# Kernel optimization log

Hardware: AMD Instinct MI355X
Metric: run time of the kernel (lower is better)

## Reference

```python
import jax, jax.numpy as jnp
import numpy as np

DOWN = 8
N_CLASSES = 80
IOU_THRESH = 0.7
ALL_ANCHORS = np.array([[10, 13], [16, 30], [33, 23], [30, 61], [62, 45],
                        [59, 119], [116, 90], [156, 198], [373, 326]],
                       np.float32) / DOWN              # anchors in grid units
ANCHOR_IDX = np.array([0, 1, 2])
ANCHORS = ALL_ANCHORS[ANCHOR_IDX]                       # [A,2]
A = 3
NC = N_CLASSES + 5


def _clog(z):
    # torch BCE clamps log at -100; double-where keeps grads finite at z==0
    safe = jnp.where(z > 0, z, 1.0)
    return jnp.where(z > 0, jnp.clip(jnp.log(safe), -100.0, None), -100.0)


def _bce_sum(p, t, w=None):
    term = t * _clog(p) + (1.0 - t) * _clog(1.0 - p)
    if w is not None:
        term = term * w
    return -jnp.sum(term)


def reference(x, targets, conv_w, conv_b):
    B, Cin, F, _ = x.shape
    T = targets.shape[1]
    anchors = jnp.asarray(ANCHORS)
    all_anchors = jnp.asarray(ALL_ANCHORS)

    # 1x1 conv + axis swap -> [B, A, Fy, Fx, NC]
    out = jnp.einsum('bchw,oc->bohw', x, conv_w) + conv_b[None, :, None, None]
    out = out.reshape(B, A, NC, F, F).transpose(0, 1, 3, 4, 2)
    sig = jax.nn.sigmoid(out)
    outputs = jnp.concatenate([sig[..., :2], out[..., 2:4], sig[..., 4:]], axis=-1)

    # decoded predicted boxes (detached), grid units
    gr = jnp.arange(F, dtype=outputs.dtype)
    grid = jnp.stack([jnp.broadcast_to(gr[None, :], (F, F)),
                      jnp.broadcast_to(gr[:, None], (F, F))], -1)   # (x,y)
    pred_xy = outputs[..., :2] + grid[None, None]
    pred_wh = jnp.exp(outputs[..., 2:4]) * anchors[None, :, None, None, :]
    pred_boxes = jax.lax.stop_gradient(jnp.concatenate([pred_xy, pred_wh], -1))

    # ground truth in grid units; valid targets are packed first (sum > 0)
    valid = jnp.sum(targets, axis=2) > 0                 # [B,T]
    n_t = jnp.sum(valid.astype(jnp.int32), axis=1)       # [B]
    gt_boxes = targets[..., :4] * F
    gt_cls = targets[..., 4].astype(jnp.int32)
    gxi = gt_boxes[..., 0].astype(jnp.int32)
    gyi = gt_boxes[..., 1].astype(jnp.int32)

    # best-matching anchor per gt (shape-only IoU vs all 9 anchors)
    wh = gt_boxes[..., 2:4]
    inter = jnp.prod(jnp.minimum(wh[:, :, None, :], all_anchors[None, None]), -1)
    union = (jnp.prod(wh, -1)[:, :, None]
             + jnp.prod(all_anchors, -1)[None, None] - inter)
    best = jnp.argmax(inter / (union + 1e-16), axis=2)   # [B,T]
    match = best[:, :, None] == jnp.asarray(ANCHOR_IDX)[None, None, :]
    keep = valid & jnp.any(match, -1)
    la = jnp.where(keep, jnp.argmax(match, -1), A)       # A == out-of-bounds -> drop

    # ignore predictions whose best IoU against any valid gt exceeds threshold
    p = pred_boxes.reshape(B, -1, 1, 4)                  # [B, A*F*F, 1, 4]
    g = gt_boxes[:, None, :, :]                          # [B, 1, T, 4]
    lo = jnp.maximum(p[..., :2] - p[..., 2:] * 0.5, g[..., :2] - g[..., 2:] * 0.5)
    hi = jnp.minimum(p[..., :2] + p[..., 2:] * 0.5, g[..., :2] + g[..., 2:] * 0.5)
    ia = jnp.prod(jnp.clip(hi - lo, 0.0, None), -1)
    iou = ia / (jnp.prod(p[..., 2:], -1) + jnp.prod(g[..., 2:], -1) - ia + 1e-16)
    iou = jnp.where(valid[:, None, :], iou, 0.0)
    high = (jnp.max(iou, -1) > IOU_THRESH).reshape(B, A, F, F).astype(outputs.dtype)
    a_rng = jnp.arange(A)
    object_mask = jnp.where(a_rng[None, :, None, None] < n_t[:, None, None, None],
                            1.0 - high, jnp.ones((), outputs.dtype))

    # scatter gt assignments (unique grid cells per image in setup -> no dup writes)
    bidx = jnp.broadcast_to(jnp.arange(B)[:, None], (B, T))
    anch = anchors[jnp.where(keep, la, 0)]               # [B,T,2]
    vals = jnp.concatenate([
        gt_boxes[..., :2] - jnp.floor(gt_boxes[..., :2]),           # frac xy
        jnp.log(gt_boxes[..., 2:4] / anch + 1e-16),                 # log wh
        jnp.ones((B, T, 1), outputs.dtype),                          # obj
        jax.nn.one_hot(gt_cls, N_CLASSES, dtype=outputs.dtype)], -1)
    scale_v = jnp.sqrt(2.0 - gt_boxes[..., 2] * gt_boxes[..., 3] / (F * F))

    tgt = jnp.zeros_like(outputs).at[bidx, la, gyi, gxi].set(vals, mode='drop')
    tmask = jnp.zeros((B, A, F, F), outputs.dtype).at[bidx, la, gyi, gxi].set(1.0, mode='drop')
    tscale = jnp.zeros((B, A, F, F), outputs.dtype).at[bidx, la, gyi, gxi].set(scale_v, mode='drop')
    object_mask = object_mask.at[bidx, la, gyi, gxi].set(1.0, mode='drop')

    tm = tmask[..., None]
    sm = tscale[..., None]
    loss_xy = _bce_sum(outputs[..., :2] * tm, tgt[..., :2] * tm, w=sm * sm)
    loss_wh = 0.5 * jnp.sum((outputs[..., 2:4] * tm * sm - tgt[..., 2:4] * tm * sm) ** 2)
    loss_obj = _bce_sum(outputs[..., 4] * object_mask, tgt[..., 4] * object_mask)
    loss_cls = _bce_sum(outputs[..., 5:] * tm, tgt[..., 5:] * tm)
    loss = loss_xy + loss_wh + loss_obj + loss_cls
    return loss, loss_xy, loss_wh, loss_obj, loss_cls


def setup_inputs():
    key = jax.random.key(0)
    k1, k2, k3 = jax.random.split(key, 3)
    B, Cin, F, T = 16, 256, 76, 50
    x = jax.random.normal(k1, (B, Cin, F, F), jnp.float32)
    conv_w = jax.random.normal(k2, (A * NC, Cin), jnp.float32) * 0.01
    conv_b = jax.random.normal(k3, (A * NC,), jnp.float32) * 0.01
    rng = np.random.default_rng(0)
    tg = np.zeros((B, T, 5), np.float32)
    for b in range(B):  # host-side data generation, not part of the op
        n = int(rng.integers(10, T + 1))
        cells = rng.choice(F * F, size=n, replace=False)   # unique grid cells
        gy, gx = cells // F, cells % F
        tg[b, :n, 0] = (gx + rng.uniform(0.05, 0.95, n)) / F
        tg[b, :n, 1] = (gy + rng.uniform(0.05, 0.95, n)) / F
        tg[b, :n, 2] = rng.uniform(0.02, 0.35, n)
        tg[b, :n, 3] = rng.uniform(0.02, 0.35, n)
        tg[b, :n, 4] = rng.integers(0, N_CLASSES, n)
    return {"x": x, "targets": jnp.asarray(tg), "conv_w": conv_w, "conv_b": conv_b}
```

## Files before the change

### kernel.cpp

```cpp
#include <hip/hip_runtime.h>
#include <math.h>

#define NB   16
#define CIN  256
#define FW   76
#define FF   (FW*FW)
#define NT   50
#define NA   3
#define NCH  85
#define POSB 256
#define NCONV ((FF + POSB - 1)/POSB)
#define CONV_BLOCKS (NB*NCONV)
#define TGT_BLOCKS  (NB*NT)
#define TOT_BLOCKS  (CONV_BLOCKS + TGT_BLOCKS)
#define KT   32
#define NCHUNK (CIN/KT)

__device__ __constant__ float c_aw[9] = {1.25f,2.0f,4.125f,3.75f,7.75f,7.375f,14.5f,19.5f,46.625f};
__device__ __constant__ float c_ah[9] = {1.625f,3.75f,2.875f,7.625f,5.625f,14.875f,11.25f,24.75f,40.75f};

__device__ inline float clogf_(float z){
  return (z > 0.f) ? fmaxf(logf(z), -100.f) : -100.f;
}
__device__ inline float sigmoidf_(float z){
  return 1.f/(1.f + expf(-z));
}

__device__ __forceinline__ void gload_lds16(const float* src, float* dst){
  __builtin_amdgcn_global_load_lds(
      (const __attribute__((address_space(1))) void*)src,
      (__attribute__((address_space(3))) void*)dst, 16, 0, 0);
}

struct TInfo {
  int valid, keep, la, gxi, gyi, cls;
  float gx, gy, gw, gh;
};

__device__ inline TInfo make_tinfo(const float* __restrict__ tg, int b, int t){
  const float* p = tg + ((size_t)b*NT + t)*5;
  float x=p[0], y=p[1], w=p[2], h=p[3], c=p[4];
  TInfo r;
  r.valid = (x+y+w+h+c) > 0.f ? 1 : 0;
  r.gx = x*(float)FW; r.gy = y*(float)FW; r.gw = w*(float)FW; r.gh = h*(float)FW;
  r.gxi = (int)r.gx; r.gyi = (int)r.gy;
  r.cls = (int)c;
  int best=0; float br=-1.f;
  #pragma unroll
  for (int i=0;i<9;++i){
    float inter = fminf(r.gw, c_aw[i]) * fminf(r.gh, c_ah[i]);
    float uni = r.gw*r.gh + c_aw[i]*c_ah[i] - inter;
    float rt = inter/(uni + 1e-16f);
    if (rt > br){ br = rt; best = i; }
  }
  r.la = best;
  r.keep = (r.valid && best < NA) ? 1 : 0;
  return r;
}

__global__ __launch_bounds__(256) void yolo_fused(
    const float* __restrict__ x, const float* __restrict__ tg,
    const float* __restrict__ W, const float* __restrict__ bias,
    double* __restrict__ part)
{
  const int bid = blockIdx.x;
  const int tid = threadIdx.x;

  if (bid < CONV_BLOCKS) {
    __shared__ float xbuf[2][KT][POSB];
    __shared__ float s_x1[NT], s_y1[NT], s_x2[NT], s_y2[NT], s_area[NT];
    __shared__ int   s_val[NT], s_code[NT];
    __shared__ int   s_nt;
    __shared__ float s_red[POSB];

    const int b    = bid / NCONV;
    const int chunk= bid % NCONV;
    const int pos0 = chunk*POSB;
    const int pos  = pos0 + tid;
    const bool act = pos < FF;

    int myvalid = 0;
    if (tid < NT) {
      TInfo ti = make_tinfo(tg, b, tid);
      myvalid = ti.valid;
      s_val[tid]  = ti.valid;
      s_x1[tid]   = ti.gx - 0.5f*ti.gw;
      s_x2[tid]   = ti.gx + 0.5f*ti.gw;
      s_y1[tid]   = ti.gy - 0.5f*ti.gh;
      s_y2[tid]   = ti.gy + 0.5f*ti.gh;
      s_area[tid] = ti.gw*ti.gh;
      s_code[tid] = ti.keep ? (ti.la*FF + ti.gyi*FW + ti.gxi) : -1;
    }
    if (tid < 64) {
      unsigned long long m = __ballot(myvalid != 0);
      if (tid == 0) s_nt = __popcll(m);
    }

    const int lane = tid & 63;
    const int w    = tid >> 6;
    int srcpos = pos0 + lane*4;
    if (srcpos > FF-4) srcpos = FF-4;
    const float* xsrc = x + (size_t)b*CIN*FF + srcpos;

    #pragma unroll
    for (int j=0;j<8;++j){
      const int krow = w*8 + j;
      gload_lds16(xsrc + (size_t)krow*FF, &xbuf[0][krow][0]);
    }
    __syncthreads();

    float acc[NA][5];
    #pragma unroll
    for (int a=0;a<NA;++a)
      #pragma unroll
      for (int c=0;c<5;++c) acc[a][c] = 0.f;

    int cb = 0;
    for (int c=0;c<NCHUNK;++c){
      if (c+1 < NCHUNK){
        const int k0n = (c+1)*KT;
        #pragma unroll
        for (int j=0;j<8;++j){
          const int krow = w*8 + j;
          gload_lds16(xsrc + (size_t)(k0n+krow)*FF, &xbuf[cb^1][krow][0]);
        }
      }
      const int k0 = c*KT;
      #pragma unroll 8
      for (int kk=0; kk<KT; ++kk){
        const float xv = xbuf[cb][kk][tid];
        const int k = k0 + kk;
        #pragma unroll
        for (int a=0;a<NA;++a)
          #pragma unroll
          for (int ch=0;ch<5;++ch)
            acc[a][ch] = fmaf(xv, W[(size_t)(a*NCH+ch)*CIN + k], acc[a][ch]);
      }
      __syncthreads();
      cb ^= 1;
    }

    float lobj = 0.f;
    if (act) {
      const int gx = pos % FW;
      const int gy = pos / FW;
      #pragma unroll
      for (int a=0;a<NA;++a) {
        const float z0 = acc[a][0] + bias[a*NCH+0];
        const float z1 = acc[a][1] + bias[a*NCH+1];
        const float z2 = acc[a][2] + bias[a*NCH+2];
        const float z3 = acc[a][3] + bias[a*NCH+3];
        const float z4 = acc[a][4] + bias[a*NCH+4];
        const float s0 = sigmoidf_(z0);
        const float s1 = sigmoidf_(z1);
        const float s4 = sigmoidf_(z4);
        const float px = s0 + (float)gx;
        const float py = s1 + (float)gy;
        const float pw = expf(z2)*c_aw[a];
        const float ph = expf(z3)*c_ah[a];
        const float px1 = px - 0.5f*pw, px2 = px + 0.5f*pw;
        const float py1 = py - 0.5f*ph, py2 = py + 0.5f*ph;
        const float parea = pw*ph;
        bool high = false, ist = false;
        const int code = a*FF + pos;
        for (int t=0;t<NT;++t) {
          if (s_val[t]) {
            float iw = fminf(px2, s_x2[t]) - fmaxf(px1, s_x1[t]); iw = fmaxf(iw, 0.f);
            float ih = fminf(py2, s_y2[t]) - fmaxf(py1, s_y1[t]); ih = fmaxf(ih, 0.f);
            float ia = iw*ih;
            float iou = ia / (parea + s_area[t] - ia + 1e-16f);
            high = high || (iou > 0.7f);
          }
          ist = ist || (s_code[t] == code);
        }
        float mask = ist ? 1.f : ((a < s_nt) ? (high ? 0.f : 1.f) : 1.f);
        if (mask != 0.f)
          lobj -= ist ? clogf_(s4) : clogf_(1.f - s4);
      }
    }

    s_red[tid] = lobj;
    __syncthreads();
    #pragma unroll
    for (int s=POSB/2; s>0; s>>=1) {
      if (tid < s) s_red[tid] += s_red[tid+s];
      __syncthreads();
    }
    if (tid == 0) {
      double* p = part + (size_t)bid*4;
      p[0] = 0.0; p[1] = 0.0; p[2] = (double)s_red[0]; p[3] = 0.0;
    }

  } else {
    const int idx = bid - CONV_BLOCKS;
    const int b = idx / NT, t = idx % NT;
    TInfo ti = make_tinfo(tg, b, t);

    __shared__ float xs[CIN];
    __shared__ float sdot[NCH*3];
    __shared__ float sxy, swh, scls;
    if (tid == 0) { sxy = 0.f; swh = 0.f; scls = 0.f; }
    __syncthreads();

    if (ti.keep) {
      const int a   = ti.la;
      const int pos = ti.gyi*FW + ti.gxi;
      if (tid < CIN) xs[tid] = x[((size_t)b*CIN + tid)*FF + pos];
      __syncthreads();

      if (tid < NCH*3) {
        const int c = tid/3, ks = tid%3;
        const int kb = ks*86;
        const int ke = (kb+86 < CIN) ? kb+86 : CIN;
        const float* __restrict__ wr = W + (size_t)(a*NCH + c)*CIN;
        float p = 0.f;
        for (int k=kb;k<ke;++k) p = fmaf(xs[k], wr[k], p);
        sdot[tid] = p;
      }
      __syncthreads();

      if (tid < NCH) {
        const float z = sdot[tid*3] + sdot[tid*3+1] + sdot[tid*3+2] + bias[a*NCH + tid];
        const float scale = sqrtf(2.f - ti.gw*ti.gh/(float)(FW*FW));
        if (tid < 2) {
          const float tv = (tid==0) ? (ti.gx - floorf(ti.gx)) : (ti.gy - floorf(ti.gy));
          const float p  = sigmoidf_(z);
          const float term = tv*clogf_(p) + (1.f-tv)*clogf_(1.f-p);
          atomicAdd(&sxy, -term*scale*scale);
        } else if (tid < 4) {
          const float anch = (tid==2) ? c_aw[a] : c_ah[a];
          const float g    = (tid==2) ? ti.gw  : ti.gh;
          const float tv   = logf(g/anch + 1e-16f);
          const float d    = (z - tv)*scale;
          atomicAdd(&swh, 0.5f*d*d);
        } else if (tid >= 5) {
          const float tv = ((tid-5) == ti.cls) ? 1.f : 0.f;
          const float p  = sigmoidf_(z);
          const float term = tv*clogf_(p) + (1.f-tv)*clogf_(1.f-p);
          atomicAdd(&scls, -term);
        }
      }
      __syncthreads();
    }

    if (tid == 0) {
      double* p = part + (size_t)bid*4;
      p[0] = (double)sxy; p[1] = (double)swh; p[2] = 0.0; p[3] = (double)scls;
    }
  }
}

__global__ void yolo_fin(const double* __restrict__ part, float* __restrict__ out){
  __shared__ double red[256];
  const int tid = threadIdx.x;
  double s = 0.0;
  for (int i = tid>>2; i < TOT_BLOCKS; i += 64)
    s += part[(size_t)i*4 + (tid&3)];
  red[tid] = s;
  __syncthreads();
  #pragma unroll
  for (int st=128; st>=4; st>>=1) {
    if (tid < st) red[tid] += red[tid+st];
    __syncthreads();
  }
  if (tid == 0) {
    float fxy  = (float)red[0];
    float fwh  = (float)red[1];
    float fobj = (float)red[2];
    float fcls = (float)red[3];
    out[0] = fxy + fwh + fobj + fcls;
    out[1] = fxy;
    out[2] = fwh;
    out[3] = fobj;
    out[4] = fcls;
  }
}

extern "C" void kernel_launch(void* const* d_in, const int* in_sizes, int n_in,
                              void* d_out, int out_size, void* d_ws, size_t ws_size,
                              hipStream_t stream) {
  const float* x    = (const float*)d_in[0];
  const float* tg   = (const float*)d_in[1];
  const float* W    = (const float*)d_in[2];
  const float* bias = (const float*)d_in[3];
  float*  out  = (float*)d_out;
  double* part = (double*)d_ws;

  hipLaunchKernelGGL(yolo_fused, dim3(TOT_BLOCKS), dim3(POSB), 0, stream,
                     x, tg, W, bias, part);
  hipLaunchKernelGGL(yolo_fin, dim3(1), dim3(256), 0, stream, part, out);
}
```

Before: 207.3 us.

## Split K across two thread halves per position and compact valid targets

Each conv block now covers 128 positions with 256 threads. The two halves of the block each reduce half of every K chunk, and the partial sums are combined through shared memory. The later IoU and objectness epilogue is spread across the halves by anchor, and the target lists are compacted with ballot and popcount so the loops visit only valid or kept targets. This doubles the number of dense blocks to raise parallelism and shorten the per-thread serial FMA chain. In exchange it adds a shared-memory reduction, an extra sync, and uneven anchor work between the halves.

```diff
diff --git a/kernel.cpp b/kernel.cpp
--- a/kernel.cpp
+++ b/kernel.cpp
@@ -8,11 +8,11 @@
 #define NT   50
 #define NA   3
 #define NCH  85
-#define POSB 256
-#define NCONV ((FF + POSB - 1)/POSB)
-#define CONV_BLOCKS (NB*NCONV)
+#define PB   128
+#define NPOSC ((FF + PB - 1)/PB)
+#define DENSE_BLOCKS (NB*NPOSC)
 #define TGT_BLOCKS  (NB*NT)
-#define TOT_BLOCKS  (CONV_BLOCKS + TGT_BLOCKS)
+#define TOT_BLOCKS  (DENSE_BLOCKS + TGT_BLOCKS)
 #define KT   32
 #define NCHUNK (CIN/KT)
 
@@ -66,46 +66,52 @@
   const int bid = blockIdx.x;
   const int tid = threadIdx.x;
 
-  if (bid < CONV_BLOCKS) {
-    __shared__ float xbuf[2][KT][POSB];
+  if (bid < DENSE_BLOCKS) {
+    __shared__ float smem[2*KT*PB];
     __shared__ float s_x1[NT], s_y1[NT], s_x2[NT], s_y2[NT], s_area[NT];
-    __shared__ int   s_val[NT], s_code[NT];
-    __shared__ int   s_nt;
-    __shared__ float s_red[POSB];
-
-    const int b    = bid / NCONV;
-    const int chunk= bid % NCONV;
-    const int pos0 = chunk*POSB;
-    const int pos  = pos0 + tid;
+    __shared__ int   s_kcode[NT];
+    __shared__ int   s_nv, s_nk;
+    __shared__ float s_red[256];
+
+    const int b    = bid / NPOSC;
+    const int pos0 = (bid % NPOSC)*PB;
+    const int p    = tid & (PB-1);
+    const int h    = tid >> 7;
+    const int pos  = pos0 + p;
     const bool act = pos < FF;
 
-    int myvalid = 0;
-    if (tid < NT) {
-      TInfo ti = make_tinfo(tg, b, tid);
-      myvalid = ti.valid;
-      s_val[tid]  = ti.valid;
-      s_x1[tid]   = ti.gx - 0.5f*ti.gw;
-      s_x2[tid]   = ti.gx + 0.5f*ti.gw;
-      s_y1[tid]   = ti.gy - 0.5f*ti.gh;
-      s_y2[tid]   = ti.gy + 0.5f*ti.gh;
-      s_area[tid] = ti.gw*ti.gh;
-      s_code[tid] = ti.keep ? (ti.la*FF + ti.gyi*FW + ti.gxi) : -1;
-    }
     if (tid < 64) {
-      unsigned long long m = __ballot(myvalid != 0);
-      if (tid == 0) s_nt = __popcll(m);
+      TInfo ti; ti.valid = 0; ti.keep = 0;
+      if (tid < NT) ti = make_tinfo(tg, b, tid);
+      unsigned long long vm = __ballot(ti.valid != 0);
+      unsigned long long km = __ballot(ti.keep  != 0);
+      unsigned long long lt = (1ull << tid) - 1ull;
+      if (ti.valid) {
+        int s = __popcll(vm & lt);
+        s_x1[s]   = ti.gx - 0.5f*ti.gw;
+        s_x2[s]   = ti.gx + 0.5f*ti.gw;
+        s_y1[s]   = ti.gy - 0.5f*ti.gh;
+        s_y2[s]   = ti.gy + 0.5f*ti.gh;
+        s_area[s] = ti.gw*ti.gh;
+      }
+      if (ti.keep) {
+        int s = __popcll(km & lt);
+        s_kcode[s] = ti.la*FF + ti.gyi*FW + ti.gxi;
+      }
+      if (tid == 0) { s_nv = __popcll(vm); s_nk = __popcll(km); }
     }
 
     const int lane = tid & 63;
-    const int w    = tid >> 6;
-    int srcpos = pos0 + lane*4;
-    if (srcpos > FF-4) srcpos = FF-4;
-    const float* xsrc = x + (size_t)b*CIN*FF + srcpos;
+    const int wv   = tid >> 6;
+    int cc = pos0 + (lane & 31)*4;
+    if (cc > FF-4) cc = FF-4;
+    const int rl = lane >> 5;
+    const float* xbase = x + (size_t)b*CIN*FF + cc;
 
     #pragma unroll
-    for (int j=0;j<8;++j){
-      const int krow = w*8 + j;
-      gload_lds16(xsrc + (size_t)krow*FF, &xbuf[0][krow][0]);
+    for (int j=0;j<4;++j){
+      const int row = wv*8 + j*2;
+      gload_lds16(xbase + (size_t)(row + rl)*FF, &smem[row*PB]);
     }
     __syncthreads();
 
@@ -119,16 +125,18 @@
     for (int c=0;c<NCHUNK;++c){
       if (c+1 < NCHUNK){
         const int k0n = (c+1)*KT;
+        const int bo  = (cb^1)*(KT*PB);
         #pragma unroll
-        for (int j=0;j<8;++j){
-          const int krow = w*8 + j;
-          gload_lds16(xsrc + (size_t)(k0n+krow)*FF, &xbuf[cb^1][krow][0]);
+        for (int j=0;j<4;++j){
+          const int row = wv*8 + j*2;
+          gload_lds16(xbase + (size_t)(k0n + row + rl)*FF, &smem[bo + row*PB]);
         }
       }
-      const int k0 = c*KT;
-      #pragma unroll 8
-      for (int kk=0; kk<KT; ++kk){
-        const float xv = xbuf[cb][kk][tid];
+      const int base = cb*(KT*PB) + (h*16)*PB + p;
+      const int k0   = c*KT + h*16;
+      #pragma unroll
+      for (int kk=0; kk<16; ++kk){
+        const float xv = smem[base + kk*PB];
         const int k = k0 + kk;
         #pragma unroll
         for (int a=0;a<NA;++a)
@@ -140,40 +148,47 @@
       cb ^= 1;
     }
 
+    #pragma unroll
+    for (int a=0;a<NA;++a)
+      #pragma unroll
+      for (int ch=0;ch<5;++ch)
+        smem[h*(15*PB) + (a*5+ch)*PB + p] = acc[a][ch];
+    __syncthreads();
+
     float lobj = 0.f;
     if (act) {
       const int gx = pos % FW;
       const int gy = pos / FW;
-      #pragma unroll
-      for (int a=0;a<NA;++a) {
-        const float z0 = acc[a][0] + bias[a*NCH+0];
-        const float z1 = acc[a][1] + bias[a*NCH+1];
-        const float z2 = acc[a][2] + bias[a*NCH+2];
-        const float z3 = acc[a][3] + bias[a*NCH+3];
-        const float z4 = acc[a][4] + bias[a*NCH+4];
-        const float s0 = sigmoidf_(z0);
-        const float s1 = sigmoidf_(z1);
-        const float s4 = sigmoidf_(z4);
+      const int a0 = (tid < 128) ? 0 : 1;
+      const int na = (tid < 128) ? 2 : 1;
+      for (int ai=0; ai<na; ++ai) {
+        const int a = a0 + ai*2;
+        float z[5];
+        #pragma unroll
+        for (int ch=0;ch<5;++ch)
+          z[ch] = smem[(a*5+ch)*PB + p] + smem[15*PB + (a*5+ch)*PB + p] + bias[a*NCH+ch];
+        const float s0 = sigmoidf_(z[0]);
+        const float s1 = sigmoidf_(z[1]);
+        const float s4 = sigmoidf_(z[4]);
         const float px = s0 + (float)gx;
         const float py = s1 + (float)gy;
-        const float pw = expf(z2)*c_aw[a];
-        const float ph = expf(z3)*c_ah[a];
+        const float pw = expf(z[2])*c_aw[a];
+        const float ph = expf(z[3])*c_ah[a];
         const float px1 = px - 0.5f*pw, px2 = px + 0.5f*pw;
         const float py1 = py - 0.5f*ph, py2 = py + 0.5f*ph;
         const float parea = pw*ph;
-        bool high = false, ist = false;
+        bool high = false;
+        for (int j=0;j<s_nv;++j) {
+          float iw = fminf(px2, s_x2[j]) - fmaxf(px1, s_x1[j]); iw = fmaxf(iw, 0.f);
+          float ih = fminf(py2, s_y2[j]) - fmaxf(py1, s_y1[j]); ih = fmaxf(ih, 0.f);
+          float ia = iw*ih;
+          float iou = ia / (parea + s_area[j] - ia + 1e-16f);
+          high = high || (iou > 0.7f);
+        }
+        bool ist = false;
         const int code = a*FF + pos;
-        for (int t=0;t<NT;++t) {
-          if (s_val[t]) {
-            float iw = fminf(px2, s_x2[t]) - fmaxf(px1, s_x1[t]); iw = fmaxf(iw, 0.f);
-            float ih = fminf(py2, s_y2[t]) - fmaxf(py1, s_y1[t]); ih = fmaxf(ih, 0.f);
-            float ia = iw*ih;
-            float iou = ia / (parea + s_area[t] - ia + 1e-16f);
-            high = high || (iou > 0.7f);
-          }
-          ist = ist || (s_code[t] == code);
-        }
-        float mask = ist ? 1.f : ((a < s_nt) ? (high ? 0.f : 1.f) : 1.f);
+        for (int j=0;j<s_nk;++j) ist = ist || (s_kcode[j] == code);
+        float mask = ist ? 1.f : ((a < s_nv) ? (high ? 0.f : 1.f) : 1.f);
         if (mask != 0.f)
           lobj -= ist ? clogf_(s4) : clogf_(1.f - s4);
       }
@@ -182,17 +197,17 @@
     s_red[tid] = lobj;
     __syncthreads();
     #pragma unroll
-    for (int s=POSB/2; s>0; s>>=1) {
+    for (int s=128; s>0; s>>=1) {
       if (tid < s) s_red[tid] += s_red[tid+s];
       __syncthreads();
     }
     if (tid == 0) {
-      double* p = part + (size_t)bid*4;
-      p[0] = 0.0; p[1] = 0.0; p[2] = (double)s_red[0]; p[3] = 0.0;
+      double* q = part + (size_t)bid*4;
+      q[0] = 0.0; q[1] = 0.0; q[2] = (double)s_red[0]; q[3] = 0.0;
     }
 
   } else {
-    const int idx = bid - CONV_BLOCKS;
+    const int idx = bid - DENSE_BLOCKS;
     const int b = idx / NT, t = idx % NT;
     TInfo ti = make_tinfo(tg, b, t);
 
@@ -213,9 +228,9 @@
         const int kb = ks*86;
         const int ke = (kb+86 < CIN) ? kb+86 : CIN;
         const float* __restrict__ wr = W + (size_t)(a*NCH + c)*CIN;
-        float p = 0.f;
-        for (int k=kb;k<ke;++k) p = fmaf(xs[k], wr[k], p);
-        sdot[tid] = p;
+        float pr = 0.f;
+        for (int k=kb;k<ke;++k) pr = fmaf(xs[k], wr[k], pr);
+        sdot[tid] = pr;
       }
       __syncthreads();
 
@@ -224,8 +239,8 @@
         const float scale = sqrtf(2.f - ti.gw*ti.gh/(float)(FW*FW));
         if (tid < 2) {
           const float tv = (tid==0) ? (ti.gx - floorf(ti.gx)) : (ti.gy - floorf(ti.gy));
-          const float p  = sigmoidf_(z);
-          const float term = tv*clogf_(p) + (1.f-tv)*clogf_(1.f-p);
+          const float pp = sigmoidf_(z);
+          const float term = tv*clogf_(pp) + (1.f-tv)*clogf_(1.f-pp);
           atomicAdd(&sxy, -term*scale*scale);
         } else if (tid < 4) {
           const float anch = (tid==2) ? c_aw[a] : c_ah[a];
@@ -235,8 +250,8 @@
           atomicAdd(&swh, 0.5f*d*d);
         } else if (tid >= 5) {
           const float tv = ((tid-5) == ti.cls) ? 1.f : 0.f;
-          const float p  = sigmoidf_(z);
-          const float term = tv*clogf_(p) + (1.f-tv)*clogf_(1.f-p);
+          const float pp = sigmoidf_(z);
+          const float term = tv*clogf_(pp) + (1.f-tv)*clogf_(1.f-pp);
           atomicAdd(&scls, -term);
         }
       }
@@ -244,8 +259,8 @@
     }
 
     if (tid == 0) {
-      double* p = part + (size_t)bid*4;
-      p[0] = (double)sxy; p[1] = (double)swh; p[2] = 0.0; p[3] = (double)scls;
+      double* q = part + (size_t)bid*4;
+      q[0] = (double)sxy; q[1] = (double)swh; q[2] = 0.0; q[3] = (double)scls;
     }
   }
 }
@@ -286,7 +301,7 @@
   float*  out  = (float*)d_out;
   double* part = (double*)d_ws;
 
-  hipLaunchKernelGGL(yolo_fused, dim3(TOT_BLOCKS), dim3(POSB), 0, stream,
+  hipLaunchKernelGGL(yolo_fused, dim3(TOT_BLOCKS), dim3(256), 0, stream,
                      x, tg, W, bias, part);
   hipLaunchKernelGGL(yolo_fin, dim3(1), dim3(256), 0, stream, part, out);
 }
```

Result: faster. 196.5 us (-5.2%).
